# Performance work log

Hardware: AMD Instinct MI355X
Metric: run time of the kernel (lower is better)

Reference implementation:

```python
import jax, jax.numpy as jnp
import numpy as np

COST_CLASS = 1.0
COST_L1 = 1.0


def _lsa(cost):
    """Exact rectangular linear sum assignment (Jonker-Volgenant / e-maxx Hungarian).
    cost: (n, m) numpy float64 with n <= m. Returns ans[n]: column assigned to each row.
    """
    n, m = cost.shape
    INF = np.inf
    u = np.zeros(n + 1)
    v = np.zeros(m + 1)
    p = np.zeros(m + 1, dtype=np.int64)    # p[j]: 1-indexed row matched to column j (0 = free)
    way = np.zeros(m + 1, dtype=np.int64)
    for i in range(1, n + 1):
        p[0] = i
        j0 = 0
        minv = np.full(m + 1, INF)
        used = np.zeros(m + 1, dtype=bool)
        while True:
            used[j0] = True
            i0 = p[j0]
            minv1 = minv[1:]               # view, in-place updates propagate
            jmask = ~used[1:]
            cur = cost[i0 - 1, :] - u[i0] - v[1:]
            upd = jmask & (cur < minv1)
            minv1[upd] = cur[upd]
            way[1:][upd] = j0
            idx = np.nonzero(jmask)[0]
            j1rel = idx[np.argmin(minv1[idx])]
            delta = minv1[j1rel]
            u[p[used]] += delta
            v[used] -= delta
            minv1[jmask] -= delta
            j0 = j1rel + 1
            if p[j0] == 0:
                break
        # augment along the alternating path
        while j0:
            j1 = way[j0]
            p[j0] = p[j1]
            j0 = j1
    ans = np.zeros(n, dtype=np.int64)
    for j in range(1, m + 1):
        if p[j] > 0:
            ans[p[j] - 1] = j - 1
    return ans


def _solve_blocks(blocks):
    """blocks: (B, Q, T) numpy. Per-batch optimal assignment, scipy-compatible output:
    row_ind sorted ascending, min(Q,T) pairs (here Q >= T so T pairs)."""
    blocks = np.asarray(blocks, dtype=np.float64)
    B, Q, T = blocks.shape
    rows = np.empty((B, T), dtype=np.int32)
    cols = np.empty((B, T), dtype=np.int32)
    for b in range(B):
        c = blocks[b]
        if Q >= T:
            ans = _lsa(c.T)                      # ans[t] = matched query q
            order = np.argsort(ans, kind="stable")
            rows[b] = ans[order]
            cols[b] = order
        else:
            ans = _lsa(c)
            rows[b] = np.arange(Q)
            cols[b] = ans
    return rows, cols


def _cost_blocks(outputs, targets):
    """Diagonal (per-sample) blocks of the DETR cost matrix.
    outputs: (B, Q, 1+P); targets: (B, T, 1+P). Returns (B, Q, T).
    Math identical to building the full (B*Q, B*T) matrix and slicing, as in the source."""
    out_prob = jax.nn.softmax(outputs[:, :, 0], axis=-1)      # softmax over the QUERY axis (as in source)
    out_pos = outputs[:, :, 1:]                                # (B, Q, P)
    tgt_pos = targets[:, :, 1:]                                # (B, T, P)
    cost_l1 = jnp.abs(out_pos[:, :, None, :] - tgt_pos[:, None, :, :]).sum(-1)  # L1 cdist, (B, Q, T)
    return COST_CLASS * (-out_prob[:, :, None]) + COST_L1 * cost_l1


def setup_inputs() -> dict:
    key = jax.random.key(0)
    k1, k2 = jax.random.split(key)
    outputs = jax.random.normal(k1, (8, 2048, 3), dtype=jnp.float32)
    targets = jax.random.uniform(k2, (8, 256, 3), dtype=jnp.float32)
    return {"outputs": outputs, "targets": targets}


def reference(outputs, targets):
    blocks = _cost_blocks(outputs, targets)                    # (B, Q, T)
    B, Q, T = blocks.shape
    n = min(Q, T)
    shapes = (jax.ShapeDtypeStruct((B, n), jnp.int32),
              jax.ShapeDtypeStruct((B, n), jnp.int32))
    row_ind, col_ind = jax.pure_callback(_solve_blocks, shapes, blocks)
    return row_ind, col_ind
```

## Files before the change

kernel.cpp:

```cpp
#include <hip/hip_runtime.h>


constexpr int B = 8;
constexpr int Q = 2048;
constexpr int T = 256;
constexpr int NT = 256;
constexpr int KPT = Q / NT;
constexpr int NW = NT / 64;
constexpr double DINF = 1e300;

struct __align__(16) CD { double u; float tx, ty; };

__device__ __forceinline__ unsigned wave_min_u32_dpp(unsigned a) {
  int v = (int)a, t;
  t = __builtin_amdgcn_update_dpp(v, v, 0x111, 0xf, 0xf, false);
  v = ((unsigned)t < (unsigned)v) ? t : v;
  t = __builtin_amdgcn_update_dpp(v, v, 0x112, 0xf, 0xf, false);
  v = ((unsigned)t < (unsigned)v) ? t : v;
  t = __builtin_amdgcn_update_dpp(v, v, 0x114, 0xf, 0xf, false);
  v = ((unsigned)t < (unsigned)v) ? t : v;
  t = __builtin_amdgcn_update_dpp(v, v, 0x118, 0xf, 0xf, false);
  v = ((unsigned)t < (unsigned)v) ? t : v;
  t = __builtin_amdgcn_update_dpp(v, v, 0x142, 0xf, 0xf, false);
  v = ((unsigned)t < (unsigned)v) ? t : v;
  t = __builtin_amdgcn_update_dpp(v, v, 0x143, 0xf, 0xf, false);
  v = ((unsigned)t < (unsigned)v) ? t : v;
  return (unsigned)__builtin_amdgcn_readlane(v, 63);
}

__launch_bounds__(NT, 1)
__global__ void hungarian_r7(const float* __restrict__ outs,
                             const float* __restrict__ tgts,
                             int* __restrict__ out) {
  const int b = blockIdx.x;
  const int tid = threadIdx.x;
  const int lane = tid & 63;
  const int wv = tid >> 6;

  __shared__ CD colDat[Q + 1];
  __shared__ CD rowDat[T + 1];
  __shared__ short p[Q + 1];
  __shared__ short visCol[T + 8];
  __shared__ double visD[T + 8];
  __shared__ uint4 pk[2][NW];
  __shared__ int ansArr[T];
  __shared__ double s_rv[NW];
  __shared__ float sh_f;

  const size_t qbase = (size_t)b * Q;
  const size_t tbase = (size_t)b * T;

  float xs[KPT], qx[KPT], qy[KPT];
#pragma unroll
  for (int k = 0; k < KPT; ++k) {
    const size_t o = (qbase + tid + k * NT) * 3;
    xs[k] = outs[o];
    qx[k] = outs[o + 1];
    qy[k] = outs[o + 2];
  }
  {
    const size_t o = (tbase + tid) * 3;
    rowDat[tid + 1].tx = tgts[o + 1];
    rowDat[tid + 1].ty = tgts[o + 2];
    rowDat[tid + 1].u = 0.0;
    if (tid == 0) { rowDat[0].tx = 0.f; rowDat[0].ty = 0.f; rowDat[0].u = 0.0; }
  }

  float lmax = xs[0];
#pragma unroll
  for (int k = 1; k < KPT; ++k) lmax = fmaxf(lmax, xs[k]);
  for (int off = 32; off > 0; off >>= 1) lmax = fmaxf(lmax, __shfl_down(lmax, off));
  if ((tid & 63) == 0) s_rv[tid >> 6] = (double)lmax;
  __syncthreads();
  if (tid == 0) {
    float m2 = (float)s_rv[0];
    for (int w = 1; w < NW; ++w) m2 = fmaxf(m2, (float)s_rv[w]);
    sh_f = m2;
  }
  __syncthreads();
  const float smax = sh_f;
  float ex[KPT];
  float lsum = 0.f;
#pragma unroll
  for (int k = 0; k < KPT; ++k) { ex[k] = expf(xs[k] - smax); lsum += ex[k]; }
  for (int off = 32; off > 0; off >>= 1) lsum += __shfl_down(lsum, off);
  if ((tid & 63) == 0) s_rv[tid >> 6] = (double)lsum;
  __syncthreads();
  if (tid == 0) {
    float s2 = 0.f;
    for (int w = 0; w < NW; ++w) s2 += (float)s_rv[w];
    sh_f = s2;
  }
  __syncthreads();
  const float ssum = sh_f;
  float np_[KPT];
#pragma unroll
  for (int k = 0; k < KPT; ++k) np_[k] = -(ex[k] / ssum);

  for (int j = tid; j <= Q; j += NT) {
    p[j] = 0;
    CD c0; c0.u = 0.0; c0.tx = -1.0f; c0.ty = 0.0f;
    colDat[j] = c0;
  }
  if (tid == 0) visCol[0] = 0;
  double vreg[KPT];
#pragma unroll
  for (int k = 0; k < KPT; ++k) vreg[k] = 0.0;
  __syncthreads();

  for (int i = 1; i <= T; ++i) {
    if (tid == 0) p[0] = (short)i;
    unsigned usedMask = 0;
    double D = 0.0;
    __syncthreads();
    double ui0 = rowDat[i].u;
    float tX = rowDat[i].tx, tY = rowDat[i].ty;
    int s = 0, S;

    for (;;) {
      double cv[KPT];
#pragma unroll
      for (int k = 0; k < KPT; ++k) {
        const float cf = fabsf(qx[k] - tX) + fabsf(qy[k] - tY) + np_[k];
        double cur = ((double)cf - ui0) - vreg[k];
        if (usedMask & (1u << k)) cur = DINF;
        cv[k] = cur;
      }
      double v0 = cv[0]; int k0 = 0;
      if (cv[1] < v0) { v0 = cv[1]; k0 = 1; }
      double v1 = cv[2]; int k1 = 2;
      if (cv[3] < v1) { v1 = cv[3]; k1 = 3; }
      double v2 = cv[4]; int k2 = 4;
      if (cv[5] < v2) { v2 = cv[5]; k2 = 5; }
      double v3 = cv[6]; int k3 = 6;
      if (cv[7] < v3) { v3 = cv[7]; k3 = 7; }
      if (v1 < v0) { v0 = v1; k0 = k1; }
      if (v3 < v2) { v2 = v3; k2 = k3; }
      double bval = v0; int bk = k0;
      if (v2 < v0) { bval = v2; bk = k2; }
      int bidx = 1 + tid + (bk << 8);

      bval += 0.0;
      const long long bb = __double_as_longlong(bval);
      const unsigned long long key = (unsigned long long)bb ^
          ((bb < 0) ? 0xFFFFFFFFFFFFFFFFull : 0x8000000000000000ull);
      const unsigned khi = (unsigned)(key >> 32);
      const unsigned klo = (unsigned)key;

      const unsigned minhi = wave_min_u32_dpp(khi);
      const unsigned long long mask = __ballot(khi == minhi);
      unsigned wklo; int widx;
      if (__popcll(mask) == 1) {
        const int wl = (int)__ffsll(mask) - 1;
        wklo = (unsigned)__builtin_amdgcn_readlane((int)klo, wl);
        widx = __builtin_amdgcn_readlane(bidx, wl);
      } else {
        wklo = 0xffffffffu; widx = 0x7fffffff;
        unsigned long long mm = mask;
        while (mm) {
          const int l = (int)__ffsll(mm) - 1; mm &= mm - 1;
          const unsigned lo2 = (unsigned)__builtin_amdgcn_readlane((int)klo, l);
          const int ix2 = __builtin_amdgcn_readlane(bidx, l);
          if (lo2 < wklo || (lo2 == wklo && ix2 < widx)) { wklo = lo2; widx = ix2; }
        }
      }
      const int par = s & 1;
      if (lane == 0) pk[par][wv] = make_uint4(minhi, wklo, (unsigned)widx, 0u);
      __syncthreads();

      const uint4 c0v = pk[par][0];
      const uint4 c1v = pk[par][1];
      const uint4 c2v = pk[par][2];
      const uint4 c3v = pk[par][3];
      const CD cd0 = colDat[(int)c0v.z];
      const CD cd1 = colDat[(int)c1v.z];
      const CD cd2 = colDat[(int)c2v.z];
      const CD cd3 = colDat[(int)c3v.z];

      unsigned long long bkk = ((unsigned long long)c0v.x << 32) | c0v.y;
      int bj = (int)c0v.z, bw = 0;
      {
        const unsigned long long k2b = ((unsigned long long)c1v.x << 32) | c1v.y;
        const int j2 = (int)c1v.z;
        if (k2b < bkk || (k2b == bkk && j2 < bj)) { bkk = k2b; bj = j2; bw = 1; }
      }
      {
        const unsigned long long k2b = ((unsigned long long)c2v.x << 32) | c2v.y;
        const int j2 = (int)c2v.z;
        if (k2b < bkk || (k2b == bkk && j2 < bj)) { bkk = k2b; bj = j2; bw = 2; }
      }
      {
        const unsigned long long k2b = ((unsigned long long)c3v.x << 32) | c3v.y;
        const int j2 = (int)c3v.z;
        if (k2b < bkk || (k2b == bkk && j2 < bj)) { bkk = k2b; bj = j2; bw = 3; }
      }
      const long long db = (long long)((bkk & 0x8000000000000000ull)
                                           ? (bkk ^ 0x8000000000000000ull) : ~bkk);
      const int j1 = bj;
      if (tid == 0) { visD[s] = D; visCol[s + 1] = (short)j1; }
      D += __longlong_as_double(db);
      if (tid == ((j1 - 1) & 255)) usedMask |= 1u << ((j1 - 1) >> 8);
      CD cd = cd0;
      if (bw == 1) cd = cd1;
      if (bw == 2) cd = cd2;
      if (bw == 3) cd = cd3;
      ++s;
      if (cd.tx < 0.0f) { S = s; break; }
      ui0 = cd.u; tX = cd.tx; tY = cd.ty;
    }

    __syncthreads();
    const double Dfin = D;
    const int rr0 = (tid < S) ? (int)p[(int)visCol[tid]] : 0;
    __syncthreads();
    if (tid < S) {
      const int cnew = (int)visCol[tid + 1];
      p[cnew] = (short)rr0;
      const double unew = rowDat[rr0].u + (Dfin - visD[tid]);
      rowDat[rr0].u = unew;
      CD cd2; cd2.u = unew; cd2.tx = rowDat[rr0].tx; cd2.ty = rowDat[rr0].ty;
      colDat[cnew] = cd2;
    }
    for (int sv = 1; sv < S; ++sv) {
      const int qv = (int)visCol[sv] - 1;
      if ((qv & 255) == tid) vreg[qv >> 8] -= (Dfin - visD[sv]);
    }
  }
  __syncthreads();

  for (int j = 1 + tid; j <= Q; j += NT) {
    const int pi = (int)p[j];
    if (pi > 0) ansArr[pi - 1] = j - 1;
  }
  __syncthreads();
  const int a = ansArr[tid];
  int rank = 0;
  for (int t2 = 0; t2 < T; ++t2) rank += (ansArr[t2] < a) ? 1 : 0;
  out[(size_t)b * T + rank] = a;
  out[(size_t)B * T + (size_t)b * T + rank] = tid;
}

extern "C" void kernel_launch(void* const* d_in, const int* in_sizes, int n_in,
                              void* d_out, int out_size, void* d_ws, size_t ws_size,
                              hipStream_t stream) {
  const float* outs = (const float*)d_in[0];
  const float* tgts = (const float*)d_in[1];
  int* out = (int*)d_out;
  hungarian_r7<<<B, NT, 0, stream>>>(outs, tgts, out);
}
```

Before: 975.1 us.

## Record augment path in registers and drop a barrier per row

Each thread whose id equals the step index now keeps that step's row, dual, target coords and distance in registers instead of thread 0 writing visD and visCol to shared memory. The augment phase then writes p, rowDat and colDat directly from those registers, which removes one __syncthreads per row and a shared-memory gather. The per-thread argmin over eight candidates is also rewritten as an fmin tree followed by equality checks. This assumes the path length S never exceeds the thread count (256), and it adds a p[j1] read on every step.

```diff
diff --git a/kernel.cpp b/kernel.cpp
--- a/kernel.cpp
+++ b/kernel.cpp
@@ -29,7 +29,7 @@
 }
 
 __launch_bounds__(NT, 1)
-__global__ void hungarian_r7(const float* __restrict__ outs,
+__global__ void hungarian_r8(const float* __restrict__ outs,
                              const float* __restrict__ tgts,
                              int* __restrict__ out) {
   const int b = blockIdx.x;
@@ -102,22 +102,25 @@
     CD c0; c0.u = 0.0; c0.tx = -1.0f; c0.ty = 0.0f;
     colDat[j] = c0;
   }
-  if (tid == 0) visCol[0] = 0;
   double vreg[KPT];
 #pragma unroll
   for (int k = 0; k < KPT; ++k) vreg[k] = 0.0;
   __syncthreads();
 
   for (int i = 1; i <= T; ++i) {
-    if (tid == 0) p[0] = (short)i;
     unsigned usedMask = 0;
     double D = 0.0;
-    __syncthreads();
+    int i0 = i;
     double ui0 = rowDat[i].u;
     float tX = rowDat[i].tx, tY = rowDat[i].ty;
     int s = 0, S;
+    int recRow = 0, recCol = 0;
+    double recU = 0.0, recD = 0.0;
+    float recTX = 0.f, recTY = 0.f;
 
     for (;;) {
+      if (tid == s) { recRow = i0; recU = ui0; recTX = tX; recTY = tY; recD = D; }
+
       double cv[KPT];
 #pragma unroll
       for (int k = 0; k < KPT; ++k) {
@@ -126,18 +129,18 @@
         if (usedMask & (1u << k)) cur = DINF;
         cv[k] = cur;
       }
-      double v0 = cv[0]; int k0 = 0;
-      if (cv[1] < v0) { v0 = cv[1]; k0 = 1; }
-      double v1 = cv[2]; int k1 = 2;
-      if (cv[3] < v1) { v1 = cv[3]; k1 = 3; }
-      double v2 = cv[4]; int k2 = 4;
-      if (cv[5] < v2) { v2 = cv[5]; k2 = 5; }
-      double v3 = cv[6]; int k3 = 6;
-      if (cv[7] < v3) { v3 = cv[7]; k3 = 7; }
-      if (v1 < v0) { v0 = v1; k0 = k1; }
-      if (v3 < v2) { v2 = v3; k2 = k3; }
-      double bval = v0; int bk = k0;
-      if (v2 < v0) { bval = v2; bk = k2; }
+      const double m01 = fmin(cv[0], cv[1]), m23 = fmin(cv[2], cv[3]);
+      const double m45 = fmin(cv[4], cv[5]), m67 = fmin(cv[6], cv[7]);
+      const double m03 = fmin(m01, m23), m47 = fmin(m45, m67);
+      double bval = fmin(m03, m47);
+      int bk = 7;
+      if (cv[6] == bval) bk = 6;
+      if (cv[5] == bval) bk = 5;
+      if (cv[4] == bval) bk = 4;
+      if (cv[3] == bval) bk = 3;
+      if (cv[2] == bval) bk = 2;
+      if (cv[1] == bval) bk = 1;
+      if (cv[0] == bval) bk = 0;
       int bidx = 1 + tid + (bk << 8);
 
       bval += 0.0;
@@ -196,31 +199,32 @@
       }
       const long long db = (long long)((bkk & 0x8000000000000000ull)
                                            ? (bkk ^ 0x8000000000000000ull) : ~bkk);
+      D += __longlong_as_double(db);
       const int j1 = bj;
-      if (tid == 0) { visD[s] = D; visCol[s + 1] = (short)j1; }
-      D += __longlong_as_double(db);
       if (tid == ((j1 - 1) & 255)) usedMask |= 1u << ((j1 - 1) >> 8);
+      if (tid == s) recCol = j1;
+      const int pj1 = (int)p[j1];
       CD cd = cd0;
       if (bw == 1) cd = cd1;
       if (bw == 2) cd = cd2;
       if (bw == 3) cd = cd3;
       ++s;
       if (cd.tx < 0.0f) { S = s; break; }
-      ui0 = cd.u; tX = cd.tx; tY = cd.ty;
+      ui0 = cd.u; tX = cd.tx; tY = cd.ty; i0 = pj1;
     }
 
     __syncthreads();
     const double Dfin = D;
-    const int rr0 = (tid < S) ? (int)p[(int)visCol[tid]] : 0;
+    if (tid < S) {
+      visCol[tid + 1] = (short)recCol;
+      visD[tid] = recD;
+      p[recCol] = (short)recRow;
+      const double unew = recU + (Dfin - recD);
+      rowDat[recRow].u = unew;
+      CD c2; c2.u = unew; c2.tx = recTX; c2.ty = recTY;
+      colDat[recCol] = c2;
+    }
     __syncthreads();
-    if (tid < S) {
-      const int cnew = (int)visCol[tid + 1];
-      p[cnew] = (short)rr0;
-      const double unew = rowDat[rr0].u + (Dfin - visD[tid]);
-      rowDat[rr0].u = unew;
-      CD cd2; cd2.u = unew; cd2.tx = rowDat[rr0].tx; cd2.ty = rowDat[rr0].ty;
-      colDat[cnew] = cd2;
-    }
     for (int sv = 1; sv < S; ++sv) {
       const int qv = (int)visCol[sv] - 1;
       if ((qv & 255) == tid) vreg[qv >> 8] -= (Dfin - visD[sv]);
@@ -246,5 +250,5 @@
   const float* outs = (const float*)d_in[0];
   const float* tgts = (const float*)d_in[1];
   int* out = (int*)d_out;
-  hungarian_r7<<<B, NT, 0, stream>>>(outs, tgts, out);
+  hungarian_r8<<<B, NT, 0, stream>>>(outs, tgts, out);
 }
```

After: 917.8 us. -5.9%, faster.
